# Kernel optimization log

Measured on AMD Instinct MI355X. Metric: run time of the kernel, lower is better.

Reference implementation:

```python
import math
import jax, jax.numpy as jnp
import numpy as np

B, S, D, H = 2, 2048, 1024, 16
HD = D // H

def setup_inputs() -> dict:
    key = jax.random.key(0)
    ks = jax.random.split(key, 5)
    scale = 1.0 / math.sqrt(D)
    return {
        "x": jax.random.normal(ks[0], (B, S, D), dtype=jnp.float32),
        "Wq": jax.random.normal(ks[1], (D, D), dtype=jnp.float32) * scale,
        "Wk": jax.random.normal(ks[2], (D, D), dtype=jnp.float32) * scale,
        "Wv": jax.random.normal(ks[3], (D, D), dtype=jnp.float32) * scale,
        "Wo": jax.random.normal(ks[4], (D, D), dtype=jnp.float32) * scale,
    }

def reference(x, Wq, Wk, Wv, Wo):
    b, s, d = x.shape
    # projections -> (b, h, s, hd)
    def split_heads(t):
        return t.reshape(b, s, H, HD).transpose(0, 2, 1, 3)
    q = split_heads(x @ Wq.T)
    k = split_heads(x @ Wk.T)
    v = split_heads(x @ Wv.T)
    scores = jnp.einsum('bhqd,bhkd->bhqk', q, k) / math.sqrt(HD)
    causal = jnp.tril(jnp.ones((s, s), dtype=bool))
    scores = jnp.where(causal, scores, -jnp.inf)
    weights = jax.nn.softmax(scores, axis=-1)
    attended = jnp.einsum('bhqk,bhkd->bhqd', weights, v)
    attended = attended.transpose(0, 2, 1, 3).reshape(b, s, d)
    return attended @ Wo.T
```

## Files before the change

### kernel.cpp

```cpp
#include <hip/hip_runtime.h>
#include <hip/hip_bf16.h>

#define Bb 2
#define Ss 2048
#define Dd 1024
#define Hh 16
#define HDd 64
#define Mm (Bb*Ss)

typedef __attribute__((ext_vector_type(8))) short short8;
typedef __attribute__((ext_vector_type(4))) float f32x4;

__device__ __forceinline__ unsigned short f2bf(float f) {
  unsigned int u = __float_as_uint(f);
  return (unsigned short)((u + 0x7FFFu + ((u >> 16) & 1u)) >> 16);
}

__device__ __forceinline__ void gload_lds16(const unsigned short* g, unsigned short* l) {
  __builtin_amdgcn_global_load_lds(
      (const __attribute__((address_space(1))) unsigned int*)g,
      (__attribute__((address_space(3))) unsigned int*)l, 16, 0, 0);
}

template<int ROWS>
__device__ __forceinline__ void stage_tile(const unsigned short* __restrict__ g, size_t ldg,
                                           unsigned short* s, int w, int lane) {
#pragma unroll
  for (int i = 0; i < ROWS / 32; ++i) {
    int c = (i * 4 + w) * 64 + lane;
    int row = c >> 3;
    int srcci = (lane & 7) ^ (row & 7);
    gload_lds16(g + (size_t)row * ldg + (srcci << 3), s + (i * 4 + w) * 512);
  }
}

__global__ __launch_bounds__(256) void cvt_all(
    const float* __restrict__ x,  const float* __restrict__ Wq,
    const float* __restrict__ Wk, const float* __restrict__ Wv,
    const float* __restrict__ Wo,
    unsigned short* __restrict__ xb, unsigned short* __restrict__ Wb,
    unsigned short* __restrict__ Wob) {
  int bid = blockIdx.x;
  const float* src; unsigned short* dst; int base;
  if (bid < 4096)      { src = x;  dst = xb;              base = bid; }
  else if (bid < 5120) { src = Wq; dst = Wb;              base = bid - 4096; }
  else if (bid < 6144) { src = Wk; dst = Wb + Dd * Dd;    base = bid - 5120; }
  else if (bid < 7168) { src = Wv; dst = Wb + 2 * Dd * Dd; base = bid - 6144; }
  else                 { src = Wo; dst = Wob;             base = bid - 7168; }
  int i = base * 256 + threadIdx.x;
  f32x4 v = ((const f32x4*)src)[i];
  ushort4 o;
  o.x = f2bf(v[0]); o.y = f2bf(v[1]); o.z = f2bf(v[2]); o.w = f2bf(v[3]);
  ((ushort4*)dst)[i] = o;
}

__global__ __launch_bounds__(256, 3) void gemm_qkv2(
    const unsigned short* __restrict__ xb,
    const unsigned short* __restrict__ Wb,
    unsigned short* __restrict__ Qo,
    unsigned short* __restrict__ Ko,
    unsigned short* __restrict__ Vt) {
  __shared__ unsigned short As[128 * 64], Bs[128 * 64];
  const int lin = (int)blockIdx.x + 32 * ((int)blockIdx.y + 8 * (int)blockIdx.z);
  const int orig = (lin & 7) * 96 + (lin >> 3);
  const int z = orig >> 8;
  const int rem = orig & 255;
  const int tm = (rem >> 3) * 128, tn = (rem & 7) * 128;
  const unsigned short* W = Wb + (size_t)z * Dd * Dd;
  const int tid = threadIdx.x, w = tid >> 6, lane = tid & 63;
  const int lrow = lane & 15, lgr = lane >> 4;
  const int wm = w >> 1, wn = w & 1;

  f32x4 acc[4][4] = {};
  for (int k0 = 0; k0 < Dd; k0 += 64) {
    stage_tile<128>(xb + (size_t)tm * Dd + k0, Dd, As, w, lane);
    stage_tile<128>(W + (size_t)tn * Dd + k0, Dd, Bs, w, lane);
    __syncthreads();
#pragma unroll
    for (int half = 0; half < 2; ++half) {
      short8 af[4], bf[4];
#pragma unroll
      for (int mt = 0; mt < 4; ++mt) {
        int row = wm * 64 + mt * 16 + lrow;
        int e = (row * 64 + half * 32 + 8 * lgr) ^ ((row & 7) << 3);
        af[mt] = *(const short8*)(As + e);
      }
#pragma unroll
      for (int nt = 0; nt < 4; ++nt) {
        int row = wn * 64 + nt * 16 + lrow;
        int e = (row * 64 + half * 32 + 8 * lgr) ^ ((row & 7) << 3);
        bf[nt] = *(const short8*)(Bs + e);
      }
      if (z != 2) {
#pragma unroll
        for (int mt = 0; mt < 4; ++mt)
#pragma unroll
          for (int nt = 0; nt < 4; ++nt)
            acc[mt][nt] = __builtin_amdgcn_mfma_f32_16x16x32_bf16(af[mt], bf[nt], acc[mt][nt], 0, 0, 0);
      } else {
#pragma unroll
        for (int mt = 0; mt < 4; ++mt)
#pragma unroll
          for (int nt = 0; nt < 4; ++nt)
            acc[mt][nt] = __builtin_amdgcn_mfma_f32_16x16x32_bf16(bf[nt], af[mt], acc[mt][nt], 0, 0, 0);
      }
    }
    __syncthreads();
  }

  if (z < 2) {
    unsigned short* C = z ? Ko : Qo;
#pragma unroll
    for (int nt = 0; nt < 4; ++nt) {
      int n = tn + wn * 64 + nt * 16 + lrow;
#pragma unroll
      for (int mt = 0; mt < 4; ++mt)
#pragma unroll
        for (int r = 0; r < 4; ++r) {
          int m = tm + wm * 64 + mt * 16 + lgr * 4 + r;
          C[(size_t)m * Dd + n] = f2bf(acc[mt][nt][r]);
        }
    }
  } else {
#pragma unroll
    for (int mt = 0; mt < 4; ++mt) {
      int m = tm + wm * 64 + mt * 16 + lrow;
      int b = m >> 11, s = m & (Ss - 1);
#pragma unroll
      for (int nt = 0; nt < 4; ++nt)
#pragma unroll
        for (int r = 0; r < 4; ++r) {
          int n = tn + wn * 64 + nt * 16 + lgr * 4 + r;
          int h = n >> 6, hd = n & (HDd - 1);
          Vt[(((size_t)(b * Hh + h)) * HDd + hd) * Ss + s] = f2bf(acc[mt][nt][r]);
        }
    }
  }
}

#define SC2 0.18033688011f
__global__ __launch_bounds__(256) void attn5(
    const unsigned short* __restrict__ Q,
    const unsigned short* __restrict__ K,
    const unsigned short* __restrict__ Vt,
    unsigned short* __restrict__ att) {
  __shared__ unsigned short Ks[2][64 * 64];
  __shared__ unsigned short Vs[2][64 * 64];
  __shared__ unsigned short Ps[4][16 * 64];

  const int lin = (int)blockIdx.x + 32 * (int)blockIdx.y;
  const int orig = (lin & 7) * 128 + (lin >> 3);
  const int bhp = orig >> 5, xq = orig & 31;
  const int b = bhp >> 4, h = bhp & (Hh - 1);
  const int t = bhp >> 1;
  const int u = (xq + 16 * t) & 31;
  const int qb = (bhp & 1) ? 31 - u : u;
  const int tid = threadIdx.x, w = tid >> 6, lane = tid & 63;
  const int lrow = lane & 15, lgr = lane >> 4;
  const int qbase = qb * 64 + w * 16;

  const unsigned short* qp = Q + (size_t)(b * Ss + qbase + lrow) * Dd + h * HDd + 8 * lgr;
  short8 aq0 = *(const short8*)qp;
  short8 aq1 = *(const short8*)(qp + 32);
  const unsigned short* Kbase = K + (size_t)(b * Ss) * Dd + h * HDd;
  const unsigned short* Vbase = Vt + (size_t)(b * Hh + h) * HDd * Ss;

  const short8 vones = {0x3F80, 0x3F80, 0x3F80, 0x3F80, 0x3F80, 0x3F80, 0x3F80, 0x3F80};
  f32x4 pacc[4] = {};
  f32x4 lacc = {};

  const int nkv = qb + 1;

  stage_tile<64>(Kbase, Dd, Ks[0], w, lane);
  stage_tile<64>(Vbase, Ss, Vs[0], w, lane);
  __syncthreads();

  for (int kvb = 0; kvb < nkv; ++kvb) {
    const int cur = kvb & 1;
    if (kvb + 1 < nkv) {
      stage_tile<64>(Kbase + (size_t)(kvb + 1) * 64 * Dd, Dd, Ks[cur ^ 1], w, lane);
      stage_tile<64>(Vbase + (size_t)(kvb + 1) * 64, Ss, Vs[cur ^ 1], w, lane);
    }
    f32x4 sacc[4] = {};
    __builtin_amdgcn_s_setprio(1);
#pragma unroll
    for (int nt = 0; nt < 4; ++nt) {
      int row = nt * 16 + lrow;
      int e0 = (row * 64 + 8 * lgr) ^ ((row & 7) << 3);
      int e1 = (row * 64 + 32 + 8 * lgr) ^ ((row & 7) << 3);
      short8 bk0 = *(const short8*)(Ks[cur] + e0);
      short8 bk1 = *(const short8*)(Ks[cur] + e1);
      sacc[nt] = __builtin_amdgcn_mfma_f32_16x16x32_bf16(aq0, bk0, sacc[nt], 0, 0, 0);
      sacc[nt] = __builtin_amdgcn_mfma_f32_16x16x32_bf16(aq1, bk1, sacc[nt], 0, 0, 0);
    }
    __builtin_amdgcn_s_setprio(0);
    if (kvb < qb) {
#pragma unroll
      for (int nt = 0; nt < 4; ++nt)
#pragma unroll
        for (int r = 0; r < 4; ++r)
          sacc[nt][r] = __builtin_amdgcn_exp2f(sacc[nt][r] * SC2);
    } else {
#pragma unroll
      for (int r = 0; r < 4; ++r) {
        int qg = qbase + lgr * 4 + r;
#pragma unroll
        for (int nt = 0; nt < 4; ++nt) {
          int kg = kvb * 64 + nt * 16 + lrow;
          float tt = sacc[nt][r] * SC2;
          sacc[nt][r] = (kg <= qg) ? __builtin_amdgcn_exp2f(tt) : 0.f;
        }
      }
    }
    unsigned short* pl = Ps[w];
#pragma unroll
    for (int nt = 0; nt < 4; ++nt)
#pragma unroll
      for (int r = 0; r < 4; ++r) {
        int row = lgr * 4 + r, col = nt * 16 + lrow;
        int byteoff = (row * 128 + col * 2) ^ ((row & 7) << 4);
        *(unsigned short*)((char*)pl + byteoff) =
            (unsigned short)(__float_as_uint(sacc[nt][r]) >> 16);
      }
    short8 apv[2];
#pragma unroll
    for (int ks = 0; ks < 2; ++ks) {
      int byteoff = (lrow * 128 + (ks * 32 + 8 * lgr) * 2) ^ ((lrow & 7) << 4);
      apv[ks] = *(const short8*)((char*)pl + byteoff);
    }
    __builtin_amdgcn_s_setprio(1);
#pragma unroll
    for (int nt = 0; nt < 4; ++nt) {
      int row = nt * 16 + lrow;
      int e0 = (row * 64 + 8 * lgr) ^ ((row & 7) << 3);
      int e1 = (row * 64 + 32 + 8 * lgr) ^ ((row & 7) << 3);
      short8 bv0 = *(const short8*)(Vs[cur] + e0);
      short8 bv1 = *(const short8*)(Vs[cur] + e1);
      pacc[nt] = __builtin_amdgcn_mfma_f32_16x16x32_bf16(apv[0], bv0, pacc[nt], 0, 0, 0);
      pacc[nt] = __builtin_amdgcn_mfma_f32_16x16x32_bf16(apv[1], bv1, pacc[nt], 0, 0, 0);
    }
    lacc = __builtin_amdgcn_mfma_f32_16x16x32_bf16(apv[0], vones, lacc, 0, 0, 0);
    lacc = __builtin_amdgcn_mfma_f32_16x16x32_bf16(apv[1], vones, lacc, 0, 0, 0);
    __builtin_amdgcn_s_setprio(0);
    __syncthreads();
  }
  float inv[4];
#pragma unroll
  for (int r = 0; r < 4; ++r) inv[r] = 1.f / lacc[r];
#pragma unroll
  for (int nt = 0; nt < 4; ++nt)
#pragma unroll
    for (int r = 0; r < 4; ++r) {
      int qg = qbase + lgr * 4 + r;
      att[(size_t)(b * Ss + qg) * Dd + h * HDd + nt * 16 + lrow] = f2bf(pacc[nt][r] * inv[r]);
    }
}

__global__ __launch_bounds__(256, 3) void gemm_o2(
    const unsigned short* __restrict__ att,
    const unsigned short* __restrict__ Wob,
    float* __restrict__ out) {
  __shared__ unsigned short As[128 * 64], Bs[64 * 64];
  const int lin = (int)blockIdx.x + 32 * (int)blockIdx.y;
  const int orig = (lin & 7) * 64 + (lin >> 3);
  const int tm = (orig >> 4) * 128, tn = (orig & 15) * 64;
  const int tid = threadIdx.x, w = tid >> 6, lane = tid & 63;
  const int lrow = lane & 15, lgr = lane >> 4;
  const int wm = w >> 1, wn = w & 1;

  f32x4 acc[4][2] = {};
  for (int k0 = 0; k0 < Dd; k0 += 64) {
    stage_tile<128>(att + (size_t)tm * Dd + k0, Dd, As, w, lane);
    stage_tile<64>(Wob + (size_t)tn * Dd + k0, Dd, Bs, w, lane);
    __syncthreads();
#pragma unroll
    for (int half = 0; half < 2; ++half) {
      short8 af[4], bf[2];
#pragma unroll
      for (int mt = 0; mt < 4; ++mt) {
        int row = wm * 64 + mt * 16 + lrow;
        int e = (row * 64 + half * 32 + 8 * lgr) ^ ((row & 7) << 3);
        af[mt] = *(const short8*)(As + e);
      }
#pragma unroll
      for (int nt = 0; nt < 2; ++nt) {
        int row = wn * 32 + nt * 16 + lrow;
        int e = (row * 64 + half * 32 + 8 * lgr) ^ ((row & 7) << 3);
        bf[nt] = *(const short8*)(Bs + e);
      }
#pragma unroll
      for (int mt = 0; mt < 4; ++mt)
#pragma unroll
        for (int nt = 0; nt < 2; ++nt)
          acc[mt][nt] = __builtin_amdgcn_mfma_f32_16x16x32_bf16(af[mt], bf[nt], acc[mt][nt], 0, 0, 0);
    }
    __syncthreads();
  }
#pragma unroll
  for (int nt = 0; nt < 2; ++nt) {
    int n = tn + wn * 32 + nt * 16 + lrow;
#pragma unroll
    for (int mt = 0; mt < 4; ++mt)
#pragma unroll
      for (int r = 0; r < 4; ++r) {
        int m = tm + wm * 64 + mt * 16 + lgr * 4 + r;
        out[(size_t)m * Dd + n] = acc[mt][nt][r];
      }
  }
}

extern "C" void kernel_launch(void* const* d_in, const int* in_sizes, int n_in,
                              void* d_out, int out_size, void* d_ws, size_t ws_size,
                              hipStream_t stream) {
  const float* x  = (const float*)d_in[0];
  const float* Wq = (const float*)d_in[1];
  const float* Wk = (const float*)d_in[2];
  const float* Wv = (const float*)d_in[3];
  const float* Wo = (const float*)d_in[4];

  char* ws = (char*)d_ws;
  unsigned short* xb  = (unsigned short*)(ws);
  unsigned short* Wb  = (unsigned short*)(ws + (8u  << 20));
  unsigned short* Wob = (unsigned short*)(ws + (14u << 20));
  unsigned short* Qb  = (unsigned short*)(ws + (16u << 20));
  unsigned short* Kb  = (unsigned short*)(ws + (24u << 20));
  unsigned short* Vt  = (unsigned short*)(ws + (32u << 20));
  unsigned short* att = xb;

  cvt_all<<<8192, 256, 0, stream>>>(x, Wq, Wk, Wv, Wo, xb, Wb, Wob);
  gemm_qkv2<<<dim3(Mm / 128, Dd / 128, 3), 256, 0, stream>>>(xb, Wb, Qb, Kb, Vt);
  attn5<<<dim3(Ss / 64, Bb * Hh), 256, 0, stream>>>(Qb, Kb, Vt, att);
  gemm_o2<<<dim3(Mm / 128, Dd / 64), 256, 0, stream>>>(att, Wob, (float*)d_out);
}
```

Baseline: 214.9 us.

## Double-buffer LDS tiles in QKV and output GEMMs and stage epilogue stores through LDS

Both projection GEMMs now keep two LDS buffers and issue the next K-tile's global-to-LDS loads before computing on the current tile. This overlaps memory latency with MFMA work and removes one barrier per iteration. The epilogues write accumulators into a padded per-wave LDS scratch and then emit 16-byte vectorized global stores, replacing scattered 2-byte and 4-byte stores. The strided V-transpose writes become contiguous along the sequence dimension. In exchange, LDS use doubles, and the QKV kernel's occupancy hint drops from 3 to 2 blocks per CU.

```diff
diff --git a/kernel.cpp b/kernel.cpp
--- a/kernel.cpp
+++ b/kernel.cpp
@@ -54,13 +54,13 @@
   ((ushort4*)dst)[i] = o;
 }
 
-__global__ __launch_bounds__(256, 3) void gemm_qkv2(
+__global__ __launch_bounds__(256, 2) void gemm_qkv2(
     const unsigned short* __restrict__ xb,
     const unsigned short* __restrict__ Wb,
     unsigned short* __restrict__ Qo,
     unsigned short* __restrict__ Ko,
     unsigned short* __restrict__ Vt) {
-  __shared__ unsigned short As[128 * 64], Bs[128 * 64];
+  __shared__ unsigned short As[2][128 * 64], Bs[2][128 * 64];
   const int lin = (int)blockIdx.x + 32 * ((int)blockIdx.y + 8 * (int)blockIdx.z);
   const int orig = (lin & 7) * 96 + (lin >> 3);
   const int z = orig >> 8;
@@ -72,10 +72,15 @@
   const int wm = w >> 1, wn = w & 1;
 
   f32x4 acc[4][4] = {};
-  for (int k0 = 0; k0 < Dd; k0 += 64) {
-    stage_tile<128>(xb + (size_t)tm * Dd + k0, Dd, As, w, lane);
-    stage_tile<128>(W + (size_t)tn * Dd + k0, Dd, Bs, w, lane);
-    __syncthreads();
+  stage_tile<128>(xb + (size_t)tm * Dd, Dd, As[0], w, lane);
+  stage_tile<128>(W + (size_t)tn * Dd, Dd, Bs[0], w, lane);
+  __syncthreads();
+  for (int k = 0; k < 16; ++k) {
+    const int cur = k & 1;
+    if (k + 1 < 16) {
+      stage_tile<128>(xb + (size_t)tm * Dd + (k + 1) * 64, Dd, As[cur ^ 1], w, lane);
+      stage_tile<128>(W + (size_t)tn * Dd + (k + 1) * 64, Dd, Bs[cur ^ 1], w, lane);
+    }
 #pragma unroll
     for (int half = 0; half < 2; ++half) {
       short8 af[4], bf[4];
@@ -83,13 +88,13 @@
       for (int mt = 0; mt < 4; ++mt) {
         int row = wm * 64 + mt * 16 + lrow;
         int e = (row * 64 + half * 32 + 8 * lgr) ^ ((row & 7) << 3);
-        af[mt] = *(const short8*)(As + e);
+        af[mt] = *(const short8*)(As[cur] + e);
       }
 #pragma unroll
       for (int nt = 0; nt < 4; ++nt) {
         int row = wn * 64 + nt * 16 + lrow;
         int e = (row * 64 + half * 32 + 8 * lgr) ^ ((row & 7) << 3);
-        bf[nt] = *(const short8*)(Bs + e);
+        bf[nt] = *(const short8*)(Bs[cur] + e);
       }
       if (z != 2) {
 #pragma unroll
@@ -108,32 +113,43 @@
     __syncthreads();
   }
 
+  unsigned short* BB = &As[0][0];
+  const int brow = lane & 15, bseg = lane >> 4;
   if (z < 2) {
     unsigned short* C = z ? Ko : Qo;
 #pragma unroll
+    for (int mt = 0; mt < 4; ++mt) {
+      unsigned short* bl = BB + (w * 2 + (mt & 1)) * (16 * 72);
+#pragma unroll
+      for (int nt = 0; nt < 4; ++nt)
+#pragma unroll
+        for (int r = 0; r < 4; ++r)
+          bl[(lgr * 4 + r) * 72 + nt * 16 + lrow] = f2bf(acc[mt][nt][r]);
+#pragma unroll
+      for (int p = 0; p < 2; ++p) {
+        short8 v = *(const short8*)(bl + brow * 72 + bseg * 8 + p * 32);
+        *(short8*)(C + (size_t)(tm + wm * 64 + mt * 16 + brow) * Dd
+                     + tn + wn * 64 + bseg * 8 + p * 32) = v;
+      }
+    }
+  } else {
+    const int bidx = tm >> 11;
+#pragma unroll
     for (int nt = 0; nt < 4; ++nt) {
-      int n = tn + wn * 64 + nt * 16 + lrow;
+      unsigned short* bl = BB + (w * 2 + (nt & 1)) * (16 * 72);
 #pragma unroll
       for (int mt = 0; mt < 4; ++mt)
 #pragma unroll
-        for (int r = 0; r < 4; ++r) {
-          int m = tm + wm * 64 + mt * 16 + lgr * 4 + r;
-          C[(size_t)m * Dd + n] = f2bf(acc[mt][nt][r]);
-        }
-    }
-  } else {
-#pragma unroll
-    for (int mt = 0; mt < 4; ++mt) {
-      int m = tm + wm * 64 + mt * 16 + lrow;
-      int b = m >> 11, s = m & (Ss - 1);
-#pragma unroll
-      for (int nt = 0; nt < 4; ++nt)
-#pragma unroll
-        for (int r = 0; r < 4; ++r) {
-          int n = tn + wn * 64 + nt * 16 + lgr * 4 + r;
-          int h = n >> 6, hd = n & (HDd - 1);
-          Vt[(((size_t)(b * Hh + h)) * HDd + hd) * Ss + s] = f2bf(acc[mt][nt][r]);
-        }
+        for (int r = 0; r < 4; ++r)
+          bl[(lgr * 4 + r) * 72 + mt * 16 + lrow] = f2bf(acc[mt][nt][r]);
+      int n = tn + wn * 64 + nt * 16 + brow;
+      int h = n >> 6, hd = n & (HDd - 1);
+#pragma unroll
+      for (int p = 0; p < 2; ++p) {
+        short8 v = *(const short8*)(bl + brow * 72 + bseg * 8 + p * 32);
+        int sbase = (tm & (Ss - 1)) + wm * 64 + bseg * 8 + p * 32;
+        *(short8*)(Vt + ((size_t)(bidx * Hh + h) * HDd + hd) * Ss + sbase) = v;
+      }
     }
   }
 }
@@ -260,7 +276,7 @@
     const unsigned short* __restrict__ att,
     const unsigned short* __restrict__ Wob,
     float* __restrict__ out) {
-  __shared__ unsigned short As[128 * 64], Bs[64 * 64];
+  __shared__ unsigned short As[2][128 * 64], Bs[2][64 * 64];
   const int lin = (int)blockIdx.x + 32 * (int)blockIdx.y;
   const int orig = (lin & 7) * 64 + (lin >> 3);
   const int tm = (orig >> 4) * 128, tn = (orig & 15) * 64;
@@ -269,10 +285,15 @@
   const int wm = w >> 1, wn = w & 1;
 
   f32x4 acc[4][2] = {};
-  for (int k0 = 0; k0 < Dd; k0 += 64) {
-    stage_tile<128>(att + (size_t)tm * Dd + k0, Dd, As, w, lane);
-    stage_tile<64>(Wob + (size_t)tn * Dd + k0, Dd, Bs, w, lane);
-    __syncthreads();
+  stage_tile<128>(att + (size_t)tm * Dd, Dd, As[0], w, lane);
+  stage_tile<64>(Wob + (size_t)tn * Dd, Dd, Bs[0], w, lane);
+  __syncthreads();
+  for (int k = 0; k < 16; ++k) {
+    const int cur = k & 1;
+    if (k + 1 < 16) {
+      stage_tile<128>(att + (size_t)tm * Dd + (k + 1) * 64, Dd, As[cur ^ 1], w, lane);
+      stage_tile<64>(Wob + (size_t)tn * Dd + (k + 1) * 64, Dd, Bs[cur ^ 1], w, lane);
+    }
 #pragma unroll
     for (int half = 0; half < 2; ++half) {
       short8 af[4], bf[2];
@@ -280,13 +301,13 @@
       for (int mt = 0; mt < 4; ++mt) {
         int row = wm * 64 + mt * 16 + lrow;
         int e = (row * 64 + half * 32 + 8 * lgr) ^ ((row & 7) << 3);
-        af[mt] = *(const short8*)(As + e);
+        af[mt] = *(const short8*)(As[cur] + e);
       }
 #pragma unroll
       for (int nt = 0; nt < 2; ++nt) {
         int row = wn * 32 + nt * 16 + lrow;
         int e = (row * 64 + half * 32 + 8 * lgr) ^ ((row & 7) << 3);
-        bf[nt] = *(const short8*)(Bs + e);
+        bf[nt] = *(const short8*)(Bs[cur] + e);
       }
 #pragma unroll
       for (int mt = 0; mt < 4; ++mt)
@@ -296,16 +317,21 @@
     }
     __syncthreads();
   }
-#pragma unroll
-  for (int nt = 0; nt < 2; ++nt) {
-    int n = tn + wn * 32 + nt * 16 + lrow;
-#pragma unroll
-    for (int mt = 0; mt < 4; ++mt)
-#pragma unroll
-      for (int r = 0; r < 4; ++r) {
-        int m = tm + wm * 64 + mt * 16 + lgr * 4 + r;
-        out[(size_t)m * Dd + n] = acc[mt][nt][r];
-      }
+  const int brow = lane & 15, bseg = lane >> 4;
+#pragma unroll
+  for (int mt = 0; mt < 4; ++mt) {
+    float* blf = ((float*)&As[0][0]) + (w * 2 + (mt & 1)) * (16 * 36);
+#pragma unroll
+    for (int nt = 0; nt < 2; ++nt)
+#pragma unroll
+      for (int r = 0; r < 4; ++r)
+        blf[(lgr * 4 + r) * 36 + nt * 16 + lrow] = acc[mt][nt][r];
+#pragma unroll
+    for (int p = 0; p < 2; ++p) {
+      f32x4 v = *(const f32x4*)(blf + brow * 36 + bseg * 4 + p * 16);
+      *(f32x4*)(out + (size_t)(tm + wm * 64 + mt * 16 + brow) * Dd
+                   + tn + wn * 32 + bseg * 4 + p * 16) = v;
+    }
   }
 }
 
```

After: 182.4 us. 1.18x faster.
